# Kernel tuning notes

Measured on AMD Instinct MI355X. Metric: run time of the kernel, lower is better.

The kernel has to match this reference:

```python
import jax, jax.numpy as jnp
import numpy as np

N_NODES = 100000
N_EDGES = 1600000
D_IN = 128
D_HID = 128
D_OUT = 128


def sage_conv(x, src, dst, W_l, b_l, W_r, n_nodes):
    # PyG SAGEConv (mean aggr): out = Linear_l(mean_j x_j) + Linear_r(x_i)
    msg = x[src]                                            # [E, d] gather
    agg = jax.ops.segment_sum(msg, dst, num_segments=n_nodes)  # [N, d]
    cnt = jax.ops.segment_sum(jnp.ones((src.shape[0],), x.dtype), dst,
                              num_segments=n_nodes)
    mean = agg / jnp.maximum(cnt, 1.0)[:, None]             # mean over neighbors
    return mean @ W_l.T + b_l + x @ W_r.T


def setup_inputs() -> dict:
    key = jax.random.key(0)
    ks = jax.random.split(key, 8)
    x = jax.random.normal(ks[0], (N_NODES, D_IN), dtype=jnp.float32)
    edge_index = jax.random.randint(ks[1], (2, N_EDGES), 0, N_NODES, dtype=jnp.int64)
    s1 = 1.0 / np.sqrt(D_IN)
    s2 = 1.0 / np.sqrt(D_HID)
    W1_l = jax.random.uniform(ks[2], (D_HID, D_IN), jnp.float32, -s1, s1)
    b1_l = jax.random.uniform(ks[3], (D_HID,), jnp.float32, -s1, s1)
    W1_r = jax.random.uniform(ks[4], (D_HID, D_IN), jnp.float32, -s1, s1)
    W2_l = jax.random.uniform(ks[5], (D_OUT, D_HID), jnp.float32, -s2, s2)
    b2_l = jax.random.uniform(ks[6], (D_OUT,), jnp.float32, -s2, s2)
    W2_r = jax.random.uniform(ks[7], (D_OUT, D_HID), jnp.float32, -s2, s2)
    return {"x": x, "edge_index": edge_index, "W1_l": W1_l, "b1_l": b1_l,
            "W1_r": W1_r, "W2_l": W2_l, "b2_l": b2_l, "W2_r": W2_r}


def reference(x, edge_index, W1_l, b1_l, W1_r, W2_l, b2_l, W2_r):
    src, dst = edge_index[0], edge_index[1]
    n = x.shape[0]
    h = sage_conv(x, src, dst, W1_l, b1_l, W1_r, n)
    h = jax.nn.relu(h)
    # F.dropout with training=False (eval mode) is identity
    out = sage_conv(h, src, dst, W2_l, b2_l, W2_r, n)
    return out
```

## Files before the change

### kernel.cpp

```cpp
#include <hip/hip_runtime.h>

typedef __attribute__((ext_vector_type(8))) short short8;
typedef __attribute__((ext_vector_type(4))) float f32x4;

#define NBMAX 512
#define CAP 8192

__device__ inline unsigned short f2bf(float f) {
  union { float f; unsigned u; } v; v.f = f;
  unsigned r = v.u + 0x7fffu + ((v.u >> 16) & 1u);
  return (unsigned short)(r >> 16);
}
__device__ inline float bf2f(unsigned short b) {
  union { unsigned u; float f; } v; v.u = ((unsigned)b) << 16;
  return v.f;
}

__device__ inline void addv8(float (&a)[8], uint4 v) {
  a[0] += bf2f((unsigned short)(v.x & 0xffffu));
  a[1] += bf2f((unsigned short)(v.x >> 16));
  a[2] += bf2f((unsigned short)(v.y & 0xffffu));
  a[3] += bf2f((unsigned short)(v.y >> 16));
  a[4] += bf2f((unsigned short)(v.z & 0xffffu));
  a[5] += bf2f((unsigned short)(v.z >> 16));
  a[6] += bf2f((unsigned short)(v.w & 0xffffu));
  a[7] += bf2f((unsigned short)(v.w >> 16));
}

__device__ inline int load_src(const int* ei, int E, int e, int f64) {
  return f64 ? ei[2 * e] : ei[e];
}
__device__ inline int load_dst(const int* ei, int E, int e, int f64) {
  return f64 ? ei[2 * (E + e)] : ei[E + e];
}

__global__ __launch_bounds__(256) void scatter2(
    const int* __restrict__ ei, int E,
    int* __restrict__ btot, int2* __restrict__ stage) {
  __shared__ int lcnt[NBMAX];
  __shared__ int lbase[NBMAX];
  __shared__ int sflag;
  const int t = threadIdx.x;
  if (t == 0) sflag = 0;
  for (int i = t; i < NBMAX; i += 256) lcnt[i] = 0;
  __syncthreads();
  const int e0 = blockIdx.x * 4096;
  {
    int e = e0 + t;
    int v = (e < E) ? ei[2 * e + 1] : 0;
    if (v) atomicOr(&sflag, 1);
  }
  __syncthreads();
  const int f64 = (sflag == 0) ? 1 : 0;

  int srcs[16], bks[16];
  int dsts[16];
#pragma unroll
  for (int i = 0; i < 16; ++i) {
    int e = e0 + i * 256 + t;
    if (e < E) {
      srcs[i] = load_src(ei, E, e, f64);
      int d = load_dst(ei, E, e, f64);
      dsts[i] = d;
      bks[i] = d >> 8;
      atomicAdd(&lcnt[d >> 8], 1);
    } else {
      bks[i] = -1;
    }
  }
  __syncthreads();
  for (int i = t; i < NBMAX; i += 256) {
    int c = lcnt[i];
    lbase[i] = c ? atomicAdd(&btot[i], c) : 0;
  }
  __syncthreads();
  for (int i = t; i < NBMAX; i += 256) lcnt[i] = 0;
  __syncthreads();
#pragma unroll
  for (int i = 0; i < 16; ++i) {
    int b = bks[i];
    if (b >= 0) {
      int r = atomicAdd(&lcnt[b], 1);
      stage[(size_t)b * CAP + lbase[b] + r] = make_int2(srcs[i], dsts[i]);
    }
  }
}

__global__ __launch_bounds__(256) void bucket_fill2(
    const int2* __restrict__ stage, const int* __restrict__ btot,
    int* __restrict__ offs, int* __restrict__ cnt, float* __restrict__ inv,
    int* __restrict__ csr, int N) {
  __shared__ int lhist[256];
  __shared__ int lscan[256];
  __shared__ int lcur[256];
  __shared__ int red[256];
  const int b = blockIdx.x;
  const int t = threadIdx.x;
  int sum = 0;
  for (int j = t; j < b; j += 256) sum += btot[j];
  red[t] = sum;
  lhist[t] = 0;
  __syncthreads();
  for (int d = 128; d; d >>= 1) {
    if (t < d) red[t] += red[t + d];
    __syncthreads();
  }
  const int base = red[0];
  const int count = btot[b];
  const int2* sp = stage + (size_t)b * CAP;
  for (int i = t; i < count; i += 256)
    atomicAdd(&lhist[sp[i].y & 255], 1);
  __syncthreads();
  int v = lhist[t];
  lscan[t] = v;
  __syncthreads();
  for (int d = 1; d < 256; d <<= 1) {
    int tv = (t >= d) ? lscan[t - d] : 0;
    __syncthreads();
    lscan[t] += tv;
    __syncthreads();
  }
  const int excl = lscan[t] - v;
  const int node = b * 256 + t;
  if (node < N) {
    offs[node] = base + excl;
    cnt[node] = v;
    inv[node] = 1.0f / (float)((v > 1) ? v : 1);
  }
  lcur[t] = base + excl;
  __syncthreads();
  for (int i = t; i < count; i += 256) {
    int2 sd = sp[i];
    int p = atomicAdd(&lcur[sd.y & 255], 1);
    csr[p] = sd.x;
  }
}

template <int AF32>
__global__ __launch_bounds__(256) void dual_gemm(
    const void* __restrict__ Av,
    const float* __restrict__ Wl, const float* __restrict__ Wr,
    unsigned short* __restrict__ Z, float* __restrict__ Y, int n) {
  __shared__ unsigned short wsh[2 * 16384];
  const int tid = threadIdx.x;

  for (int mi = 0; mi < 2; ++mi) {
    const float* W = mi ? Wr : Wl;
#pragma unroll
    for (int it = 0; it < 8; ++it) {
      int id = it * 256 + tid;
      int j = id >> 4;
      int kc = id & 15;
      int s = kc >> 2, q = kc & 3;
      int jt = j >> 4, nn2 = j & 15;
      int c = (s * 8 + jt) * 4 + q;
      const float* src = W + j * 128 + kc * 8;
      union { unsigned short u[8]; uint4 v; } t;
#pragma unroll
      for (int k = 0; k < 8; ++k) t.u[k] = f2bf(src[k]);
      *(uint4*)(wsh + mi * 16384 + (c * 16 + nn2) * 8) = t.v;
    }
  }
  __syncthreads();

  const int lane = tid & 63;
  const int wave = tid >> 6;
  const int nn = lane & 15;
  const int quad = lane >> 4;
  const int rowbase = blockIdx.x * 64 + wave * 16;

  int nodeA = rowbase + nn;
  if (nodeA > n - 1) nodeA = n - 1;

  short8 a[4];
#pragma unroll
  for (int s = 0; s < 4; ++s) {
    if (AF32) {
      const float* ap = (const float*)Av + (size_t)nodeA * 128 + s * 32 + quad * 8;
      union { unsigned short u[8]; short8 v; } t;
#pragma unroll
      for (int k = 0; k < 8; ++k) t.u[k] = f2bf(ap[k]);
      a[s] = t.v;
    } else {
      a[s] = *(const short8*)((const unsigned short*)Av + (size_t)nodeA * 128 + s * 32 + quad * 8);
    }
  }

  f32x4 accl[8], accr[8];
#pragma unroll
  for (int jt = 0; jt < 8; ++jt) {
    accl[jt] = (f32x4){0.f, 0.f, 0.f, 0.f};
    accr[jt] = (f32x4){0.f, 0.f, 0.f, 0.f};
  }

#pragma unroll
  for (int jt = 0; jt < 8; ++jt) {
#pragma unroll
    for (int s = 0; s < 4; ++s) {
      int c = (s * 8 + jt) * 4 + quad;
      short8 bl = *(const short8*)(wsh + (c * 16 + nn) * 8);
      short8 br = *(const short8*)(wsh + 16384 + (c * 16 + nn) * 8);
      accl[jt] = __builtin_amdgcn_mfma_f32_16x16x32_bf16(a[s], bl, accl[jt], 0, 0, 0);
      accr[jt] = __builtin_amdgcn_mfma_f32_16x16x32_bf16(a[s], br, accr[jt], 0, 0, 0);
    }
  }

#pragma unroll
  for (int jt = 0; jt < 8; ++jt) {
#pragma unroll
    for (int r = 0; r < 4; ++r) {
      int ro = rowbase + quad * 4 + r;
      if (ro < n) {
        int col = jt * 16 + nn;
        Y[(size_t)ro * 128 + col] = accr[jt][r];
        Z[(size_t)ro * 128 + col] = f2bf(accl[jt][r]);
      }
    }
  }
}

template <int RELU, int OUTBF>
__global__ __launch_bounds__(256, 4) void agg_fuse2(
    const unsigned short* __restrict__ Z, const float* Ybuf,
    const float* __restrict__ bias, const float* __restrict__ inv,
    const int* __restrict__ offs, const int* __restrict__ cnt,
    const int* __restrict__ csr, void* outp, int n) {
  int pr = (int)((blockIdx.x * 256 + threadIdx.x) >> 6);
  int n0 = pr * 2;
  if (n0 >= n) return;
  const int n1 = n0 + 1;
  const bool has1 = (n1 < n);
  const int lane = threadIdx.x & 63;
  const int g = lane >> 4;
  const int l = lane & 15;
  const int deg0 = cnt[n0];
  const int deg1 = has1 ? cnt[n1] : 0;
  const int start = offs[n0];
  const int T = deg0 + deg1;
  float acc0[8] = {0.f, 0.f, 0.f, 0.f, 0.f, 0.f, 0.f, 0.f};
  float acc1[8] = {0.f, 0.f, 0.f, 0.f, 0.f, 0.f, 0.f, 0.f};

  if (T <= 64) {
    int idx = (lane < T) ? csr[start + lane] : 0;
    int jmax = (T + 3) >> 2;
#pragma unroll 8
    for (int j = 0; j < jmax; ++j) {
      int e = j * 4 + g;
      int nbv = __shfl(idx, e);
      if (e < T) {
        uint4 v = *(const uint4*)(Z + (size_t)nbv * 128 + l * 8);
        if (e < deg0) addv8(acc0, v);
        else addv8(acc1, v);
      }
    }
  } else {
    for (int node = 0; node < 2; ++node) {
      int dg = node ? deg1 : deg0;
      int st = node ? (start + deg0) : start;
      for (int base = 0; base < dg; base += 64) {
        int m = dg - base;
        if (m > 64) m = 64;
        int idx = (lane < m) ? csr[st + base + lane] : 0;
#pragma unroll 4
        for (int i = 0; i < m; i += 4) {
          int sl = i + g;
          int nbv = __shfl(idx, sl & 63);
          if (sl < m) {
            uint4 v = *(const uint4*)(Z + (size_t)nbv * 128 + l * 8);
            if (node) addv8(acc1, v);
            else addv8(acc0, v);
          }
        }
      }
    }
  }

#pragma unroll
  for (int j = 0; j < 8; ++j) {
    acc0[j] += __shfl_xor(acc0[j], 16);
    acc0[j] += __shfl_xor(acc0[j], 32);
    acc1[j] += __shfl_xor(acc1[j], 16);
    acc1[j] += __shfl_xor(acc1[j], 32);
  }

  const int c0 = l * 8 + g * 2;
  const float bv0 = bias[c0], bv1 = bias[c0 + 1];

  {
    float s = inv[n0];
    float2 yv = *(const float2*)(Ybuf + (size_t)n0 * 128 + c0);
    float o0 = fmaf(acc0[g * 2 + 0], s, bv0 + yv.x);
    float o1 = fmaf(acc0[g * 2 + 1], s, bv1 + yv.y);
    if (RELU) { o0 = fmaxf(o0, 0.f); o1 = fmaxf(o1, 0.f); }
    if (OUTBF) {
      unsigned pkt = (unsigned)f2bf(o0) | ((unsigned)f2bf(o1) << 16);
      *(unsigned*)((unsigned short*)outp + (size_t)n0 * 128 + c0) = pkt;
    } else {
      *(float2*)((float*)outp + (size_t)n0 * 128 + c0) = make_float2(o0, o1);
    }
  }
  if (has1) {
    float s = inv[n1];
    float2 yv = *(const float2*)(Ybuf + (size_t)n1 * 128 + c0);
    float o0 = fmaf(acc1[g * 2 + 0], s, bv0 + yv.x);
    float o1 = fmaf(acc1[g * 2 + 1], s, bv1 + yv.y);
    if (RELU) { o0 = fmaxf(o0, 0.f); o1 = fmaxf(o1, 0.f); }
    if (OUTBF) {
      unsigned pkt = (unsigned)f2bf(o0) | ((unsigned)f2bf(o1) << 16);
      *(unsigned*)((unsigned short*)outp + (size_t)n1 * 128 + c0) = pkt;
    } else {
      *(float2*)((float*)outp + (size_t)n1 * 128 + c0) = make_float2(o0, o1);
    }
  }
}


extern "C" void kernel_launch(void* const* d_in, const int* in_sizes, int n_in,
                              void* d_out, int out_size, void* d_ws, size_t ws_size,
                              hipStream_t stream) {
  const float* x = (const float*)d_in[0];
  const int* ei = (const int*)d_in[1];
  const float* W1l = (const float*)d_in[2];
  const float* b1 = (const float*)d_in[3];
  const float* W1r = (const float*)d_in[4];
  const float* W2l = (const float*)d_in[5];
  const float* b2 = (const float*)d_in[6];
  const float* W2r = (const float*)d_in[7];
  float* out = (float*)d_out;

  const int N = in_sizes[0] / 128;
  const int E = in_sizes[1] / 2;
  const int nb = (N + 255) / 256;

  char* p = (char*)d_ws;
  auto alloc = [&](size_t bytes) {
    char* r = p;
    p += (bytes + 255) & ~(size_t)255;
    return r;
  };
  int* btot = (int*)alloc((size_t)NBMAX * 4);
  int* cnt = (int*)alloc((size_t)N * 4);
  int* offs = (int*)alloc((size_t)N * 4);
  float* inv = (float*)alloc((size_t)N * 4);
  int* csr = (int*)alloc((size_t)E * 4);
  unsigned short* zb = (unsigned short*)alloc((size_t)N * 128 * 2);
  size_t stage_bytes = (size_t)nb * CAP * 8;
  size_t hb_bytes = (size_t)N * 128 * 2;
  char* shared_region = alloc(stage_bytes > hb_bytes ? stage_bytes : hb_bytes);
  unsigned short* hb = (unsigned short*)shared_region;
  int2* stage = (int2*)shared_region;

  hipMemsetAsync(btot, 0, (size_t)nb * 4, stream);

  scatter2<<<(E + 4095) / 4096, 256, 0, stream>>>(ei, E, btot, stage);
  bucket_fill2<<<nb, 256, 0, stream>>>(stage, btot, offs, cnt, inv, csr, N);

  const int gb = (N + 63) / 64;
  const int pairs = (N + 1) / 2;
  const int ab2 = (pairs + 3) / 4;

  dual_gemm<1><<<gb, 256, 0, stream>>>((const void*)x, W1l, W1r, zb, out, N);
  agg_fuse2<1, 1><<<ab2, 256, 0, stream>>>(zb, out, b1, inv, offs, cnt, csr, (void*)hb, N);
  dual_gemm<0><<<gb, 256, 0, stream>>>((const void*)hb, W2l, W2r, zb, out, N);
  agg_fuse2<0, 0><<<ab2, 256, 0, stream>>>(zb, out, b2, inv, offs, cnt, csr, (void*)out, N);
}
```

Baseline: 338.2 us.

## Aggregate neighbor features before the linear transform instead of after

Each SAGE layer is reordered to compute the neighbor mean first (gathering bf16 features) and then run one fused GEMM over [mean, self] with bias and ReLU applied in its epilogue. A separate cast kernel converts x to bf16 up front, staged in the output buffer. This drops the fp32 Y intermediate and its write-then-read round trip, which cuts global memory traffic per layer. In exchange it adds an extra kernel launch, and the mean is rounded to bf16 before the GEMM, which may change numerics slightly.

```diff
diff --git a/kernel.cpp b/kernel.cpp
--- a/kernel.cpp
+++ b/kernel.cpp
@@ -32,6 +32,22 @@
 }
 __device__ inline int load_dst(const int* ei, int E, int e, int f64) {
   return f64 ? ei[2 * (E + e)] : ei[E + e];
+}
+
+__global__ __launch_bounds__(256) void castbf(
+    const float* __restrict__ x, unsigned short* __restrict__ xb, int n8) {
+  int i = blockIdx.x * 256 + threadIdx.x;
+  const int stride = gridDim.x * 256;
+  for (; i < n8; i += stride) {
+    float4 v0 = ((const float4*)x)[2 * i];
+    float4 v1 = ((const float4*)x)[2 * i + 1];
+    union { unsigned short u[8]; uint4 v; } t;
+    t.u[0] = f2bf(v0.x); t.u[1] = f2bf(v0.y);
+    t.u[2] = f2bf(v0.z); t.u[3] = f2bf(v0.w);
+    t.u[4] = f2bf(v1.x); t.u[5] = f2bf(v1.y);
+    t.u[6] = f2bf(v1.z); t.u[7] = f2bf(v1.w);
+    ((uint4*)xb)[i] = t.v;
+  }
 }
 
 __global__ __launch_bounds__(256) void scatter2(
@@ -136,95 +152,10 @@
   }
 }
 
-template <int AF32>
-__global__ __launch_bounds__(256) void dual_gemm(
-    const void* __restrict__ Av,
-    const float* __restrict__ Wl, const float* __restrict__ Wr,
-    unsigned short* __restrict__ Z, float* __restrict__ Y, int n) {
-  __shared__ unsigned short wsh[2 * 16384];
-  const int tid = threadIdx.x;
-
-  for (int mi = 0; mi < 2; ++mi) {
-    const float* W = mi ? Wr : Wl;
-#pragma unroll
-    for (int it = 0; it < 8; ++it) {
-      int id = it * 256 + tid;
-      int j = id >> 4;
-      int kc = id & 15;
-      int s = kc >> 2, q = kc & 3;
-      int jt = j >> 4, nn2 = j & 15;
-      int c = (s * 8 + jt) * 4 + q;
-      const float* src = W + j * 128 + kc * 8;
-      union { unsigned short u[8]; uint4 v; } t;
-#pragma unroll
-      for (int k = 0; k < 8; ++k) t.u[k] = f2bf(src[k]);
-      *(uint4*)(wsh + mi * 16384 + (c * 16 + nn2) * 8) = t.v;
-    }
-  }
-  __syncthreads();
-
-  const int lane = tid & 63;
-  const int wave = tid >> 6;
-  const int nn = lane & 15;
-  const int quad = lane >> 4;
-  const int rowbase = blockIdx.x * 64 + wave * 16;
-
-  int nodeA = rowbase + nn;
-  if (nodeA > n - 1) nodeA = n - 1;
-
-  short8 a[4];
-#pragma unroll
-  for (int s = 0; s < 4; ++s) {
-    if (AF32) {
-      const float* ap = (const float*)Av + (size_t)nodeA * 128 + s * 32 + quad * 8;
-      union { unsigned short u[8]; short8 v; } t;
-#pragma unroll
-      for (int k = 0; k < 8; ++k) t.u[k] = f2bf(ap[k]);
-      a[s] = t.v;
-    } else {
-      a[s] = *(const short8*)((const unsigned short*)Av + (size_t)nodeA * 128 + s * 32 + quad * 8);
-    }
-  }
-
-  f32x4 accl[8], accr[8];
-#pragma unroll
-  for (int jt = 0; jt < 8; ++jt) {
-    accl[jt] = (f32x4){0.f, 0.f, 0.f, 0.f};
-    accr[jt] = (f32x4){0.f, 0.f, 0.f, 0.f};
-  }
-
-#pragma unroll
-  for (int jt = 0; jt < 8; ++jt) {
-#pragma unroll
-    for (int s = 0; s < 4; ++s) {
-      int c = (s * 8 + jt) * 4 + quad;
-      short8 bl = *(const short8*)(wsh + (c * 16 + nn) * 8);
-      short8 br = *(const short8*)(wsh + 16384 + (c * 16 + nn) * 8);
-      accl[jt] = __builtin_amdgcn_mfma_f32_16x16x32_bf16(a[s], bl, accl[jt], 0, 0, 0);
-      accr[jt] = __builtin_amdgcn_mfma_f32_16x16x32_bf16(a[s], br, accr[jt], 0, 0, 0);
-    }
-  }
-
-#pragma unroll
-  for (int jt = 0; jt < 8; ++jt) {
-#pragma unroll
-    for (int r = 0; r < 4; ++r) {
-      int ro = rowbase + quad * 4 + r;
-      if (ro < n) {
-        int col = jt * 16 + nn;
-        Y[(size_t)ro * 128 + col] = accr[jt][r];
-        Z[(size_t)ro * 128 + col] = f2bf(accl[jt][r]);
-      }
-    }
-  }
-}
-
-template <int RELU, int OUTBF>
-__global__ __launch_bounds__(256, 4) void agg_fuse2(
-    const unsigned short* __restrict__ Z, const float* Ybuf,
-    const float* __restrict__ bias, const float* __restrict__ inv,
+__global__ __launch_bounds__(256, 4) void agg_mean(
+    const unsigned short* __restrict__ A, const float* __restrict__ inv,
     const int* __restrict__ offs, const int* __restrict__ cnt,
-    const int* __restrict__ csr, void* outp, int n) {
+    const int* __restrict__ csr, unsigned short* __restrict__ M, int n) {
   int pr = (int)((blockIdx.x * 256 + threadIdx.x) >> 6);
   int n0 = pr * 2;
   if (n0 >= n) return;
@@ -248,7 +179,7 @@
       int e = j * 4 + g;
       int nbv = __shfl(idx, e);
       if (e < T) {
-        uint4 v = *(const uint4*)(Z + (size_t)nbv * 128 + l * 8);
+        uint4 v = *(const uint4*)(A + (size_t)nbv * 128 + l * 8);
         if (e < deg0) addv8(acc0, v);
         else addv8(acc1, v);
       }
@@ -266,7 +197,7 @@
           int sl = i + g;
           int nbv = __shfl(idx, sl & 63);
           if (sl < m) {
-            uint4 v = *(const uint4*)(Z + (size_t)nbv * 128 + l * 8);
+            uint4 v = *(const uint4*)(A + (size_t)nbv * 128 + l * 8);
             if (node) addv8(acc1, v);
             else addv8(acc0, v);
           }
@@ -284,32 +215,96 @@
   }
 
   const int c0 = l * 8 + g * 2;
-  const float bv0 = bias[c0], bv1 = bias[c0 + 1];
-
   {
     float s = inv[n0];
-    float2 yv = *(const float2*)(Ybuf + (size_t)n0 * 128 + c0);
-    float o0 = fmaf(acc0[g * 2 + 0], s, bv0 + yv.x);
-    float o1 = fmaf(acc0[g * 2 + 1], s, bv1 + yv.y);
-    if (RELU) { o0 = fmaxf(o0, 0.f); o1 = fmaxf(o1, 0.f); }
-    if (OUTBF) {
-      unsigned pkt = (unsigned)f2bf(o0) | ((unsigned)f2bf(o1) << 16);
-      *(unsigned*)((unsigned short*)outp + (size_t)n0 * 128 + c0) = pkt;
-    } else {
-      *(float2*)((float*)outp + (size_t)n0 * 128 + c0) = make_float2(o0, o1);
-    }
+    unsigned pkt = (unsigned)f2bf(acc0[g * 2 + 0] * s) |
+                   ((unsigned)f2bf(acc0[g * 2 + 1] * s) << 16);
+    *(unsigned*)(M + (size_t)n0 * 128 + c0) = pkt;
   }
   if (has1) {
     float s = inv[n1];
-    float2 yv = *(const float2*)(Ybuf + (size_t)n1 * 128 + c0);
-    float o0 = fmaf(acc1[g * 2 + 0], s, bv0 + yv.x);
-    float o1 = fmaf(acc1[g * 2 + 1], s, bv1 + yv.y);
-    if (RELU) { o0 = fmaxf(o0, 0.f); o1 = fmaxf(o1, 0.f); }
-    if (OUTBF) {
-      unsigned pkt = (unsigned)f2bf(o0) | ((unsigned)f2bf(o1) << 16);
-      *(unsigned*)((unsigned short*)outp + (size_t)n1 * 128 + c0) = pkt;
-    } else {
-      *(float2*)((float*)outp + (size_t)n1 * 128 + c0) = make_float2(o0, o1);
+    unsigned pkt = (unsigned)f2bf(acc1[g * 2 + 0] * s) |
+                   ((unsigned)f2bf(acc1[g * 2 + 1] * s) << 16);
+    *(unsigned*)(M + (size_t)n1 * 128 + c0) = pkt;
+  }
+}
+
+template <int RELU, int OUTBF>
+__global__ __launch_bounds__(256) void gemm_fused(
+    const unsigned short* __restrict__ Am,
+    const unsigned short* __restrict__ As,
+    const float* __restrict__ Wl, const float* __restrict__ Wr,
+    const float* __restrict__ bias, void* __restrict__ outp, int n) {
+  __shared__ unsigned short wsh[2 * 16384];
+  const int tid = threadIdx.x;
+
+  for (int mi = 0; mi < 2; ++mi) {
+    const float* W = mi ? Wr : Wl;
+#pragma unroll
+    for (int it = 0; it < 8; ++it) {
+      int id = it * 256 + tid;
+      int j = id >> 4;
+      int kc = id & 15;
+      int s = kc >> 2, q = kc & 3;
+      int jt = j >> 4, nn2 = j & 15;
+      int c = (s * 8 + jt) * 4 + q;
+      const float* src = W + j * 128 + kc * 8;
+      union { unsigned short u[8]; uint4 v; } t;
+#pragma unroll
+      for (int k = 0; k < 8; ++k) t.u[k] = f2bf(src[k]);
+      *(uint4*)(wsh + mi * 16384 + (c * 16 + nn2) * 8) = t.v;
+    }
+  }
+  __syncthreads();
+
+  const int lane = tid & 63;
+  const int wave = tid >> 6;
+  const int nn = lane & 15;
+  const int quad = lane >> 4;
+  const int rowbase = blockIdx.x * 64 + wave * 16;
+
+  int nodeA = rowbase + nn;
+  if (nodeA > n - 1) nodeA = n - 1;
+
+  short8 am[4], asf[4];
+#pragma unroll
+  for (int s = 0; s < 4; ++s) {
+    am[s] = *(const short8*)(Am + (size_t)nodeA * 128 + s * 32 + quad * 8);
+    asf[s] = *(const short8*)(As + (size_t)nodeA * 128 + s * 32 + quad * 8);
+  }
+
+  f32x4 acc[8];
+#pragma unroll
+  for (int jt = 0; jt < 8; ++jt) acc[jt] = (f32x4){0.f, 0.f, 0.f, 0.f};
+
+#pragma unroll
+  for (int jt = 0; jt < 8; ++jt) {
+#pragma unroll
+    for (int s = 0; s < 4; ++s) {
+      int c = (s * 8 + jt) * 4 + quad;
+      short8 bl = *(const short8*)(wsh + (c * 16 + nn) * 8);
+      short8 br = *(const short8*)(wsh + 16384 + (c * 16 + nn) * 8);
+      acc[jt] = __builtin_amdgcn_mfma_f32_16x16x32_bf16(am[s], bl, acc[jt], 0, 0, 0);
+      acc[jt] = __builtin_amdgcn_mfma_f32_16x16x32_bf16(asf[s], br, acc[jt], 0, 0, 0);
+    }
+  }
+
+#pragma unroll
+  for (int jt = 0; jt < 8; ++jt) {
+    int col = jt * 16 + nn;
+    float bv = bias[col];
+#pragma unroll
+    for (int r = 0; r < 4; ++r) {
+      int ro = rowbase + quad * 4 + r;
+      if (ro < n) {
+        float o = acc[jt][r] + bv;
+        if (RELU) o = fmaxf(o, 0.f);
+        if (OUTBF) {
+          ((unsigned short*)outp)[(size_t)ro * 128 + col] = f2bf(o);
+        } else {
+          ((float*)outp)[(size_t)ro * 128 + col] = o;
+        }
+      }
     }
   }
 }
@@ -343,15 +338,18 @@
   int* offs = (int*)alloc((size_t)N * 4);
   float* inv = (float*)alloc((size_t)N * 4);
   int* csr = (int*)alloc((size_t)E * 4);
-  unsigned short* zb = (unsigned short*)alloc((size_t)N * 128 * 2);
+  unsigned short* Mb = (unsigned short*)alloc((size_t)N * 128 * 2);
   size_t stage_bytes = (size_t)nb * CAP * 8;
   size_t hb_bytes = (size_t)N * 128 * 2;
   char* shared_region = alloc(stage_bytes > hb_bytes ? stage_bytes : hb_bytes);
   unsigned short* hb = (unsigned short*)shared_region;
   int2* stage = (int2*)shared_region;
 
+  unsigned short* xb = (unsigned short*)d_out;
+
   hipMemsetAsync(btot, 0, (size_t)nb * 4, stream);
 
+  castbf<<<2048, 256, 0, stream>>>(x, xb, N * 128 / 8);
   scatter2<<<(E + 4095) / 4096, 256, 0, stream>>>(ei, E, btot, stage);
   bucket_fill2<<<nb, 256, 0, stream>>>(stage, btot, offs, cnt, inv, csr, N);
 
@@ -359,8 +357,8 @@
   const int pairs = (N + 1) / 2;
   const int ab2 = (pairs + 3) / 4;
 
-  dual_gemm<1><<<gb, 256, 0, stream>>>((const void*)x, W1l, W1r, zb, out, N);
-  agg_fuse2<1, 1><<<ab2, 256, 0, stream>>>(zb, out, b1, inv, offs, cnt, csr, (void*)hb, N);
-  dual_gemm<0><<<gb, 256, 0, stream>>>((const void*)hb, W2l, W2r, zb, out, N);
-  agg_fuse2<0, 0><<<ab2, 256, 0, stream>>>(zb, out, b2, inv, offs, cnt, csr, (void*)out, N);
-}
+  agg_mean<<<ab2, 256, 0, stream>>>(xb, inv, offs, cnt, csr, Mb, N);
+  gemm_fused<1, 1><<<gb, 256, 0, stream>>>(Mb, xb, W1l, W1r, b1, (void*)hb, N);
+  agg_mean<<<ab2, 256, 0, stream>>>(hb, inv, offs, cnt, csr, Mb, N);
+  gemm_fused<0, 0><<<gb, 256, 0, stream>>>(Mb, hb, W2l, W2r, b2, (void*)out, N);
+}
```

Result: slower. 356.2 us (+5.3%).
